# Optimization experiments

Hardware: AMD Instinct MI355X
Metric: run time of the kernel (lower is better)

Reference implementation:

```python
import jax, jax.numpy as jnp
import numpy as np

H = 24  # hidden size hard-coded in TrendGRU


def setup_inputs() -> dict:
    key = jax.random.key(0)
    ks = jax.random.split(key, 7)
    B, T = 32768, 512
    s_ih = 1.0 / np.sqrt(H)
    x = jax.random.normal(ks[0], (B, T, 1), dtype=jnp.float32)
    # GRUCell params (PyTorch layout: rows ordered r, z, n)
    W_ih = jax.random.uniform(ks[1], (3 * H, 1), minval=-s_ih, maxval=s_ih, dtype=jnp.float32)
    W_hh = jax.random.uniform(ks[2], (3 * H, H), minval=-s_ih, maxval=s_ih, dtype=jnp.float32)
    b_ih = jax.random.uniform(ks[3], (3 * H,), minval=-s_ih, maxval=s_ih, dtype=jnp.float32)
    b_hh = jax.random.uniform(ks[4], (3 * H,), minval=-s_ih, maxval=s_ih, dtype=jnp.float32)
    fc_w = jax.random.uniform(ks[5], (2, H), minval=-s_ih, maxval=s_ih, dtype=jnp.float32)
    fc_b = jax.random.uniform(ks[6], (2,), minval=-s_ih, maxval=s_ih, dtype=jnp.float32)
    return {"x": x, "W_ih": W_ih, "b_ih": b_ih, "W_hh": W_hh, "b_hh": b_hh,
            "fc_w": fc_w, "fc_b": fc_b}


def _gru_scan(x, W_ih, b_ih, W_hh, b_hh):
    B = x.shape[0]
    # precompute input projections for all timesteps: (B,T,1)@(1,3H) -> (T,B,3H)
    gx = jnp.einsum('bti,gi->tbg', x, W_ih) + b_ih
    h0 = jnp.zeros((B, H), dtype=x.dtype)

    def step(h, gx_t):
        gh = h @ W_hh.T + b_hh                      # (B, 3H)
        xr, xz, xn = jnp.split(gx_t, 3, axis=-1)    # PyTorch order r, z, n
        hr, hz, hn = jnp.split(gh, 3, axis=-1)
        r = jax.nn.sigmoid(xr + hr)
        z = jax.nn.sigmoid(xz + hz)
        n = jnp.tanh(xn + r * hn)
        h_new = (1.0 - z) * n + z * h
        return h_new, None

    h_final, _ = jax.lax.scan(step, h0, gx)
    return h_final


def reference(x, W_ih, b_ih, W_hh, b_hh, fc_w, fc_b):
    h = _gru_scan(x, W_ih, b_ih, W_hh, b_hh)
    return h @ fc_w.T + fc_b  # (B, 2)
```

## Files before the change

### kernel.cpp

```cpp
#include <hip/hip_runtime.h>


#define GRU_T 512
#define HS 40
#define FS 28

typedef __attribute__((ext_vector_type(8)))  short bf16x8;
typedef __attribute__((ext_vector_type(16))) float f32x16;

__device__ __forceinline__ float bf16hi_f(float v) {
    unsigned u = __float_as_uint(v);
    u = (u + 0x7FFFu + ((u >> 16) & 1u)) & 0xFFFF0000u;
    return __uint_as_float(u);
}
__device__ __forceinline__ unsigned bf16_rne(float v) {
    unsigned u = __float_as_uint(v);
    return (u + 0x7FFFu + ((u >> 16) & 1u)) >> 16;
}
__device__ __forceinline__ float sigf(float a) {
    return __builtin_amdgcn_rcpf(1.0f + __builtin_amdgcn_exp2f(-a));
}
__device__ __forceinline__ float tnhf(float v) {
    return fmaf(-2.0f, __builtin_amdgcn_rcpf(1.0f + __builtin_amdgcn_exp2f(v)), 1.0f);
}
__device__ __forceinline__ f32x16 mfma32(bf16x8 a, bf16x8 b, f32x16 c) {
    return __builtin_amdgcn_mfma_f32_32x32x16_bf16(a, b, c, 0, 0, 0);
}

__global__ __launch_bounds__(64) void trend_gru_mfma32(
    const float* __restrict__ x,
    const float* __restrict__ W_ih,
    const float* __restrict__ b_ih,
    const float* __restrict__ W_hh,
    const float* __restrict__ b_hh,
    const float* __restrict__ fc_w,
    const float* __restrict__ fc_b,
    float* __restrict__ out)
{
    const int lane = threadIdx.x;
    const int e    = lane & 31;
    const int half = lane >> 5;
    const int elem0 = blockIdx.x * 32;

    __shared__ __align__(16) unsigned short Hlds[32 * HS];
    __shared__ __align__(16) float Flds[32 * FS];

    const float L2E = 1.4426950408889634f;

    bf16x8 A[3][2][2];
#pragma unroll
    for (int g = 0; g < 3; ++g) {
        const float sc = (g == 2) ? 2.0f * L2E : L2E;
        const int m = e;
        const bool valid = m < 24;
        const int R = g * 24 + (valid ? m : 0);
        const float wx = (g < 2 && valid) ? sc * W_ih[R] : 0.0f;
        const float bb = valid ? sc * ((g < 2) ? (b_ih[R] + b_hh[R]) : b_hh[R]) : 0.0f;
        const float wxh = bf16hi_f(wx), bbh = bf16hi_f(bb);
#pragma unroll
        for (int s = 0; s < 2; ++s) {
            bf16x8 fh, fl;
#pragma unroll
            for (int jj = 0; jj < 8; ++jj) {
                const int k = s * 16 + half * 8 + jj;
                float vh = 0.0f, vl = 0.0f;
                if (valid && k < 24) {
                    const float w  = sc * W_hh[R * 24 + k];
                    const float wh = bf16hi_f(w);
                    vh = wh; vl = w - wh;
                } else if (valid) {
                    if (k == 24 || k == 25)      vh = wxh;
                    else if (k == 26)            vh = wx - wxh;
                    else if (k == 27)            vh = bbh;
                    else if (k == 28)            vh = bb - bbh;
                }
                fh[jj] = (short)bf16_rne(vh);
                fl[jj] = (short)bf16_rne(vl);
            }
            A[g][s][0] = fh;
            A[g][s][1] = fl;
        }
    }

    float wn_s[12], bn_s[12];
#pragma unroll
    for (int s = 0; s < 12; ++s) {
        const int j = (s & 3) + 8 * (s >> 2) + 4 * half;
        wn_s[s] = 2.0f * L2E * W_ih[48 + j];
        bn_s[s] = 2.0f * L2E * b_ih[48 + j];
    }

    {
        uint2 z2; z2.x = 0; z2.y = 0;
#pragma unroll
        for (int G = 0; G < 3; ++G)
            *(uint2*)(&Hlds[e * HS + G * 8 + half * 4]) = z2;
    }

    const float* xp = x + (size_t)(elem0 + e) * GRU_T;
    float xv = xp[0];

    float h[12];
#pragma unroll
    for (int s = 0; s < 12; ++s) h[s] = 0.0f;

    const f32x16 z16 = {0.f,0.f,0.f,0.f,0.f,0.f,0.f,0.f,
                        0.f,0.f,0.f,0.f,0.f,0.f,0.f,0.f};

#pragma unroll 1
    for (int t = 0; t < GRU_T; ++t) {
        const bf16x8 B0 = *(const bf16x8*)(&Hlds[e * HS + half * 8]);
        bf16x8 B1 = *(const bf16x8*)(&Hlds[e * HS + 16]);
        {
            const unsigned uhi = bf16_rne(xv);
            const float xh = __uint_as_float(uhi << 16);
            const unsigned ulo = bf16_rne(xv - xh);
            uint4 xq;
            xq.x = uhi | (ulo << 16);
            xq.y = uhi | 0x3F800000u;
            xq.z = 0x00003F80u;
            xq.w = 0;
            if (half) B1 = *(bf16x8*)&xq;
        }
        const float xnext = xp[(t + 1 < GRU_T) ? t + 1 : t];

        f32x16 aR = mfma32(A[0][0][0], B0, z16);
        aR = mfma32(A[0][0][1], B0, aR);
        aR = mfma32(A[0][1][0], B1, aR);
        aR = mfma32(A[0][1][1], B1, aR);
        f32x16 aZ = mfma32(A[1][0][0], B0, z16);
        aZ = mfma32(A[1][0][1], B0, aZ);
        aZ = mfma32(A[1][1][0], B1, aZ);
        aZ = mfma32(A[1][1][1], B1, aZ);
        f32x16 aN = mfma32(A[2][0][0], B0, z16);
        aN = mfma32(A[2][0][1], B0, aN);
        aN = mfma32(A[2][1][0], B1, aN);
        aN = mfma32(A[2][1][1], B1, aN);

#pragma unroll
        for (int G = 0; G < 3; ++G) {
            unsigned u4[4];
#pragma unroll
            for (int q = 0; q < 4; ++q) {
                const int s = G * 4 + q;
                const float rr  = sigf(aR[s]);
                const float zz  = sigf(aZ[s]);
                const float aXv = fmaf(wn_s[s], xv, bn_s[s]);
                const float nn  = tnhf(fmaf(rr, aN[s], aXv));
                const float hn  = fmaf(zz, h[s] - nn, nn);
                h[s] = hn;
                unsigned u = __float_as_uint(hn);
                u4[q] = u + 0x7FFFu + ((u >> 16) & 1u);
            }
            uint2 d;
            d.x = __builtin_amdgcn_perm(u4[1], u4[0], 0x07060302u);
            d.y = __builtin_amdgcn_perm(u4[3], u4[2], 0x07060302u);
            *(uint2*)(&Hlds[e * HS + G * 8 + half * 4]) = d;
        }
        xv = xnext;
    }

#pragma unroll
    for (int G = 0; G < 3; ++G) {
        float4 f4;
        f4.x = h[G * 4 + 0]; f4.y = h[G * 4 + 1];
        f4.z = h[G * 4 + 2]; f4.w = h[G * 4 + 3];
        *(float4*)(&Flds[e * FS + G * 8 + half * 4]) = f4;
    }
    if (lane < 32) {
        float o0 = fc_b[0], o1 = fc_b[1];
#pragma unroll
        for (int j = 0; j < 24; ++j) {
            const float hv = Flds[lane * FS + j];
            o0 = fmaf(hv, fc_w[j],      o0);
            o1 = fmaf(hv, fc_w[24 + j], o1);
        }
        float2 o; o.x = o0; o.y = o1;
        *(float2*)(out + (size_t)(elem0 + lane) * 2) = o;
    }
}

extern "C" void kernel_launch(void* const* d_in, const int* in_sizes, int n_in,
                              void* d_out, int out_size, void* d_ws, size_t ws_size,
                              hipStream_t stream) {
    const float* x    = (const float*)d_in[0];
    const float* W_ih = (const float*)d_in[1];
    const float* b_ih = (const float*)d_in[2];
    const float* W_hh = (const float*)d_in[3];
    const float* b_hh = (const float*)d_in[4];
    const float* fc_w = (const float*)d_in[5];
    const float* fc_b = (const float*)d_in[6];
    float* out = (float*)d_out;

    const int B = in_sizes[0] / GRU_T;
    const int grid = B / 32;
    trend_gru_mfma32<<<grid, 64, 0, stream>>>(x, W_ih, b_ih, W_hh, b_hh,
                                              fc_w, fc_b, out);
}
```

Measured before the change: 476.9 us.

## Exchange GRU hidden state via permlane32 swaps instead of LDS round-trip

```diff
diff --git a/kernel.cpp b/kernel.cpp
--- a/kernel.cpp
+++ b/kernel.cpp
@@ -2,11 +2,11 @@
 
 
 #define GRU_T 512
-#define HS 40
 #define FS 28
 
 typedef __attribute__((ext_vector_type(8)))  short bf16x8;
 typedef __attribute__((ext_vector_type(16))) float f32x16;
+typedef __attribute__((ext_vector_type(2)))  unsigned uint2v;
 
 __device__ __forceinline__ float bf16hi_f(float v) {
     unsigned u = __float_as_uint(v);
@@ -17,8 +17,10 @@
     unsigned u = __float_as_uint(v);
     return (u + 0x7FFFu + ((u >> 16) & 1u)) >> 16;
 }
-__device__ __forceinline__ float sigf(float a) {
-    return __builtin_amdgcn_rcpf(1.0f + __builtin_amdgcn_exp2f(-a));
+__device__ __forceinline__ unsigned cvt_pk_bf16(float lo, float hi) {
+    unsigned r;
+    asm("v_cvt_pk_bf16_f32 %0, %1, %2" : "=v"(r) : "v"(lo), "v"(hi));
+    return r;
 }
 __device__ __forceinline__ float tnhf(float v) {
     return fmaf(-2.0f, __builtin_amdgcn_rcpf(1.0f + __builtin_amdgcn_exp2f(v)), 1.0f);
@@ -42,7 +44,6 @@
     const int half = lane >> 5;
     const int elem0 = blockIdx.x * 32;
 
-    __shared__ __align__(16) unsigned short Hlds[32 * HS];
     __shared__ __align__(16) float Flds[32 * FS];
 
     const float L2E = 1.4426950408889634f;
@@ -90,13 +91,6 @@
         bn_s[s] = 2.0f * L2E * b_ih[48 + j];
     }
 
-    {
-        uint2 z2; z2.x = 0; z2.y = 0;
-#pragma unroll
-        for (int G = 0; G < 3; ++G)
-            *(uint2*)(&Hlds[e * HS + G * 8 + half * 4]) = z2;
-    }
-
     const float* xp = x + (size_t)(elem0 + e) * GRU_T;
     float xv = xp[0];
 
@@ -104,24 +98,39 @@
 #pragma unroll
     for (int s = 0; s < 12; ++s) h[s] = 0.0f;
 
+    unsigned P0 = 0, P1 = 0, P2 = 0, P3 = 0, P4 = 0, P5 = 0;
+
     const f32x16 z16 = {0.f,0.f,0.f,0.f,0.f,0.f,0.f,0.f,
                         0.f,0.f,0.f,0.f,0.f,0.f,0.f,0.f};
 
 #pragma unroll 1
     for (int t = 0; t < GRU_T; ++t) {
-        const bf16x8 B0 = *(const bf16x8*)(&Hlds[e * HS + half * 8]);
-        bf16x8 B1 = *(const bf16x8*)(&Hlds[e * HS + 16]);
-        {
-            const unsigned uhi = bf16_rne(xv);
-            const float xh = __uint_as_float(uhi << 16);
-            const unsigned ulo = bf16_rne(xv - xh);
-            uint4 xq;
-            xq.x = uhi | (ulo << 16);
-            xq.y = uhi | 0x3F800000u;
-            xq.z = 0x00003F80u;
-            xq.w = 0;
-            if (half) B1 = *(bf16x8*)&xq;
-        }
+        const uint2v r02 = __builtin_amdgcn_permlane32_swap(P0, P2, false, false);
+        const uint2v r13 = __builtin_amdgcn_permlane32_swap(P1, P3, false, false);
+        uint4 b0q;
+        b0q.x = r02.x;
+        b0q.y = r13.x;
+        b0q.z = r02.y;
+        b0q.w = r13.y;
+
+        const uint2v r44 = __builtin_amdgcn_permlane32_swap(P4, P4, false, false);
+        const uint2v r55 = __builtin_amdgcn_permlane32_swap(P5, P5, false, false);
+        uint4 b1q;
+        b1q.x = P4;
+        b1q.y = P5;
+        b1q.z = r44.y;
+        b1q.w = r55.y;
+        if (half) {
+            const unsigned xy = cvt_pk_bf16(xv, 1.0f);
+            const float    xh = __uint_as_float(xy << 16);
+            const unsigned xx = cvt_pk_bf16(xv, xv - xh);
+            b1q.x = xx;
+            b1q.y = xy;
+            b1q.z = 0x00003F80u;
+            b1q.w = 0u;
+        }
+        const bf16x8 B0 = *(const bf16x8*)&b0q;
+        const bf16x8 B1 = *(const bf16x8*)&b1q;
         const float xnext = xp[(t + 1 < GRU_T) ? t + 1 : t];
 
         f32x16 aR = mfma32(A[0][0][0], B0, z16);
@@ -139,23 +148,27 @@
 
 #pragma unroll
         for (int G = 0; G < 3; ++G) {
-            unsigned u4[4];
+            float hv[4];
 #pragma unroll
             for (int q = 0; q < 4; ++q) {
                 const int s = G * 4 + q;
-                const float rr  = sigf(aR[s]);
-                const float zz  = sigf(aZ[s]);
+                const float er = __builtin_amdgcn_exp2f(-aR[s]);
+                const float ez = __builtin_amdgcn_exp2f(-aZ[s]);
+                const float dr = 1.0f + er, dz = 1.0f + ez;
+                const float qi = __builtin_amdgcn_rcpf(dr * dz);
+                const float rr = qi * dz;
+                const float zz = qi * dr;
                 const float aXv = fmaf(wn_s[s], xv, bn_s[s]);
                 const float nn  = tnhf(fmaf(rr, aN[s], aXv));
                 const float hn  = fmaf(zz, h[s] - nn, nn);
                 h[s] = hn;
-                unsigned u = __float_as_uint(hn);
-                u4[q] = u + 0x7FFFu + ((u >> 16) & 1u);
+                hv[q] = hn;
             }
-            uint2 d;
-            d.x = __builtin_amdgcn_perm(u4[1], u4[0], 0x07060302u);
-            d.y = __builtin_amdgcn_perm(u4[3], u4[2], 0x07060302u);
-            *(uint2*)(&Hlds[e * HS + G * 8 + half * 4]) = d;
+            const unsigned pa = cvt_pk_bf16(hv[0], hv[1]);
+            const unsigned pb = cvt_pk_bf16(hv[2], hv[3]);
+            if (G == 0)      { P0 = pa; P1 = pb; }
+            else if (G == 1) { P2 = pa; P3 = pb; }
+            else             { P4 = pa; P5 = pb; }
         }
         xv = xnext;
     }
```

New measurement: 475.4 us. About the same (-0.3%).
